# Kernel optimization log

Hardware: AMD Instinct MI355X
Metric: run time of the kernel (lower is better)

## Reference

```python
import jax, jax.numpy as jnp
import numpy as np

B, H, W = 16, 512, 512


def conv2d(x, w, b):
    # NCHW conv, stride 1, padding 1 (SAME for 3x3)
    y = jax.lax.conv_general_dilated(
        x, w, window_strides=(1, 1), padding=((1, 1), (1, 1)),
        dimension_numbers=("NCHW", "OIHW", "NCHW"))
    return y + b[None, :, None, None]


def bilinear_sample(img, py, px):
    # img: [B,H,W]; py,px: [B,K,H,W] float sample coords. Zero padding outside.
    Hh, Ww = img.shape[1], img.shape[2]
    y0 = jnp.floor(py)
    x0 = jnp.floor(px)
    wy = py - y0  # fractional weights
    wx = px - x0
    y0i = y0.astype(jnp.int32)
    x0i = x0.astype(jnp.int32)

    def gather(yi, xi):
        valid = (yi >= 0) & (yi < Hh) & (xi >= 0) & (xi < Ww)
        yc = jnp.clip(yi, 0, Hh - 1)
        xc = jnp.clip(xi, 0, Ww - 1)
        v = jax.vmap(lambda im, yy, xx: im[yy, xx])(img, yc, xc)
        return jnp.where(valid, v, jnp.zeros((), img.dtype))

    v00 = gather(y0i, x0i)
    v01 = gather(y0i, x0i + 1)
    v10 = gather(y0i + 1, x0i)
    v11 = gather(y0i + 1, x0i + 1)
    return (v00 * (1 - wy) * (1 - wx) + v01 * (1 - wy) * wx
            + v10 * wy * (1 - wx) + v11 * wy * wx)


def setup_inputs() -> dict:
    key = jax.random.key(0)
    ks = jax.random.split(key, 7)
    pm25 = jax.random.normal(ks[0], (B, 1, H, W), jnp.float32)
    avg_wind = jax.random.normal(ks[1], (B, 2, H, W), jnp.float32)
    topo = jax.random.normal(ks[2], (B, 1, H, W), jnp.float32)
    # offset_conv params (Kaiming-ish small random)
    conv1_w = jax.random.normal(ks[3], (16, 3, 3, 3), jnp.float32) * (1.0 / np.sqrt(3 * 9))
    conv1_b = jax.random.normal(ks[4], (16,), jnp.float32) * 0.01
    conv2_w = jax.random.normal(ks[5], (18, 16, 3, 3), jnp.float32) * (1.0 / np.sqrt(16 * 9))
    conv2_b = jax.random.normal(ks[6], (18,), jnp.float32) * 0.01
    # dirac init: identity 3x3 kernel
    weight = jnp.zeros((1, 1, 3, 3), jnp.float32).at[0, 0, 1, 1].set(1.0)
    return {"pm25": pm25, "avg_wind": avg_wind, "topo": topo,
            "conv1_w": conv1_w, "conv1_b": conv1_b,
            "conv2_w": conv2_w, "conv2_b": conv2_b, "weight": weight}


def reference(pm25, avg_wind, topo, conv1_w, conv1_b, conv2_w, conv2_b, weight):
    # offset-predicting conv stack
    feat = jax.nn.gelu(conv2d(jnp.concatenate([avg_wind, topo], axis=1), conv1_w, conv1_b), approximate=False)
    offsets = conv2d(feat, conv2_w, conv2_b)          # [B, 2*3*3, H, W]
    b, _, h, w = offsets.shape
    off = offsets.reshape(b, 9, 2, h, w)              # k = i*3 + j; [.,k,0]=dy, [.,k,1]=dx
    dy, dx = off[:, :, 0], off[:, :, 1]               # [B,9,H,W]

    ys = jnp.arange(h, dtype=pm25.dtype)[None, None, :, None]
    xs = jnp.arange(w, dtype=pm25.dtype)[None, None, None, :]
    ki = jnp.arange(3, dtype=pm25.dtype)
    kdy = (jnp.repeat(ki, 3) - 1.0)[None, :, None, None]  # kernel row offset - pad
    kdx = (jnp.tile(ki, 3) - 1.0)[None, :, None, None]    # kernel col offset - pad

    py = ys + kdy + dy                                # sample rows   [B,9,H,W]
    px = xs + kdx + dx                                # sample cols   [B,9,H,W]

    samp = bilinear_sample(pm25[:, 0], py, px)        # [B,9,H,W]
    wk = weight.reshape(9)                            # single-channel 3x3 kernel
    out = jnp.einsum("bkhw,k->bhw", samp, wk)[:, None]
    return out                                        # [B,1,H,W]
```

## Files before the change

kernel.cpp:

```cpp
#include <hip/hip_runtime.h>
#include <math.h>

#define Bn 16
#define Hh 512
#define Ww 512
#define HW_ (Hh * Ww)
#define TW 32
#define TH 16
#define NTHREADS 512
#define S 37
#define NROWS 20
#define SIN_N 800
#define NFP 672
#define NT 42

typedef __bf16 bfrag __attribute__((ext_vector_type(8)));
typedef __bf16 bf4   __attribute__((ext_vector_type(4)));
typedef float  ffrag __attribute__((ext_vector_type(16)));
typedef float  f32x4 __attribute__((ext_vector_type(4)));
typedef float  f32x2 __attribute__((ext_vector_type(2)));

__device__ __forceinline__ short f2bf(float f) {
    unsigned u = __float_as_uint(f);
    unsigned r = u + 0x7FFFu + ((u >> 16) & 1u);
    return (short)(r >> 16);
}

__device__ __forceinline__ f32x2 mk2(float a, float b) { f32x2 t; t.x = a; t.y = b; return t; }

__device__ __forceinline__ f32x2 gelu_fast2(f32x2 x) {
    const float C0 = 1.1259890f, C1 = -0.3565430f, C2 = 0.0848830f,
                C3 = -0.0110610f, C4 = 0.0005820f;
    f32x2 y = x * 0.70710678f;
    f32x2 t;
    t.x = fminf(fmaxf(y.x, -2.5f), 2.5f);
    t.y = fminf(fmaxf(y.y, -2.5f), 2.5f);
    f32x2 u = t * t;
    f32x2 p = u * C4 + C3;
    p = p * u + C2;
    p = p * u + C1;
    p = p * u + C0;
    f32x2 e = t * p;
    f32x2 h = x * 0.5f;
    return h * e + h;
}

__device__ __forceinline__ float bilin(const float* __restrict__ img, float py, float px) {
    float y0f = floorf(py), x0f = floorf(px);
    float wy = py - y0f, wx = px - x0f;
    int y0 = (int)y0f, x0 = (int)x0f;
    int yc0 = min(max(y0, 0), Hh - 1), yc1 = min(max(y0 + 1, 0), Hh - 1);
    int xc0 = min(max(x0, 0), Ww - 1), xc1 = min(max(x0 + 1, 0), Ww - 1);
    bool vy0 = (unsigned)y0 < (unsigned)Hh, vy1 = (unsigned)(y0 + 1) < (unsigned)Hh;
    bool vx0 = (unsigned)x0 < (unsigned)Ww, vx1 = (unsigned)(x0 + 1) < (unsigned)Ww;
    const float* r0 = img + yc0 * Ww;
    const float* r1 = img + yc1 * Ww;
    float v00 = (vy0 && vx0) ? r0[xc0] : 0.0f;
    float v01 = (vy0 && vx1) ? r0[xc1] : 0.0f;
    float v10 = (vy1 && vx0) ? r1[xc0] : 0.0f;
    float v11 = (vy1 && vx1) ? r1[xc1] : 0.0f;
    return (1.0f - wy) * ((1.0f - wx) * v00 + wx * v01) +
           wy          * ((1.0f - wx) * v10 + wx * v11);
}

__global__ void pack_w(const float* __restrict__ w2, const float* __restrict__ w1,
                       const float* __restrict__ b1, int* __restrict__ ws) {
    const int lane = threadIdx.x;
    const int l31  = lane & 31;
    const int lh   = lane >> 5;
    for (int tap = 0; tap < 9; ++tap) {
        int pk[4];
        #pragma unroll
        for (int jj = 0; jj < 4; ++jj) {
            float v0 = (l31 < 18) ? w2[(l31 * 16 + lh * 8 + 2 * jj    ) * 9 + tap] : 0.0f;
            float v1 = (l31 < 18) ? w2[(l31 * 16 + lh * 8 + 2 * jj + 1) * 9 + tap] : 0.0f;
            pk[jj] = ((int)(unsigned short)f2bf(v0)) | ((int)f2bf(v1) << 16);
        }
        ((int4*)ws)[tap * 64 + lane] = make_int4(pk[0], pk[1], pk[2], pk[3]);
    }
    const int m  = lane & 15;
    const int kq = lane >> 4;
    for (int t = 0; t < 2; ++t) {
        int pk[4];
        #pragma unroll
        for (int jj = 0; jj < 4; ++jj) {
            float vv[2];
            #pragma unroll
            for (int h = 0; h < 2; ++h) {
                int k   = kq * 8 + 2 * jj + h;
                int kyl = k >> 4, kx = (k >> 2) & 3, c = k & 3;
                int ky  = 2 * t + kyl;
                float x = 0.0f;
                if (kx < 3 && c < 3 && ky < 3) x = w1[m * 27 + c * 9 + ky * 3 + kx];
                if (t == 0 && k == 3) x = b1[m];
                vv[h] = x;
            }
            pk[jj] = ((int)(unsigned short)f2bf(vv[0])) | ((int)f2bf(vv[1]) << 16);
        }
        ((int4*)ws)[576 + t * 64 + lane] = make_int4(pk[0], pk[1], pk[2], pk[3]);
    }
}

#define SMEM_BYTES (SIN_N * 16 + 2 * NFP * 16)

__global__ __launch_bounds__(NTHREADS, 8) void residual_advection_fused(
    const float* __restrict__ pm25,
    const float* __restrict__ wind,
    const float* __restrict__ topo,
    const float* __restrict__ b2,
    const float* __restrict__ wt,
    const int*   __restrict__ wsB,
    float* __restrict__ out)
{
    __shared__ __align__(16) char smem[SMEM_BYTES];
    __bf16* s_in   = (__bf16*)smem;
    __bf16* s_feat = (__bf16*)(smem + SIN_N * 16);

    const int tid = threadIdx.x;
    const int bb  = blockIdx.z;
    const int ty0 = blockIdx.y * TH;
    const int tx0 = blockIdx.x * TW;
    const bool edge = (ty0 == 0) || (ty0 == Hh - TH) || (tx0 == 0) || (tx0 == Ww - TW);

    const int lane = tid & 63;
    const int wv   = tid >> 6;
    const int l31  = lane & 31;
    const int lh   = lane >> 5;

    const bfrag* WF = (const bfrag*)wsB;

    bfrag w1f0 = WF[576 + lane];
    bfrag w1f1 = WF[640 + lane];

    for (int idx = tid; idx < SIN_N; idx += NTHREADS) {
        float c0 = 0.0f, c1 = 0.0f, c2 = 0.0f;
        if (idx < NROWS * S) {
            int r = idx / S, c = idx - r * S;
            if (!edge) {
                int g = (ty0 - 2 + r) * Ww + (tx0 - 2 + c);
                c0 = wind[(bb * 2 + 0) * HW_ + g];
                c1 = wind[(bb * 2 + 1) * HW_ + g];
                c2 = topo[bb * HW_ + g];
            } else {
                int gy = ty0 - 2 + r, gx = tx0 - 2 + c;
                if ((unsigned)gy < (unsigned)Hh && (unsigned)gx < (unsigned)Ww) {
                    int g = gy * Ww + gx;
                    c0 = wind[(bb * 2 + 0) * HW_ + g];
                    c1 = wind[(bb * 2 + 1) * HW_ + g];
                    c2 = topo[bb * HW_ + g];
                }
            }
        }
        bf4 v;
        v[0] = (__bf16)c0; v[1] = (__bf16)c1; v[2] = (__bf16)c2; v[3] = (__bf16)1.0f;
        *(bf4*)&s_in[idx * 8] = v;
        if (idx > 0) *(bf4*)&s_in[idx * 8 - 4] = v;
    }
    __syncthreads();

    {
        const int n    = lane & 15;
        const int kq   = lane >> 4;
        const int qoff = (kq >> 1) * S + (kq & 1) * 2;
        for (int tt = wv; tt < NT; tt += 8) {
            const int p = tt * 16 + n;
            f32x4 acc;
            acc[0] = 0.0f; acc[1] = 0.0f; acc[2] = 0.0f; acc[3] = 0.0f;
            bfrag bx0 = *(const bfrag*)&s_in[(p + qoff) * 8];
            bfrag bx1 = *(const bfrag*)&s_in[(p + qoff + 2 * S) * 8];
            acc = __builtin_amdgcn_mfma_f32_16x16x32_bf16(w1f0, bx0, acc, 0, 0, 0);
            acc = __builtin_amdgcn_mfma_f32_16x16x32_bf16(w1f1, bx1, acc, 0, 0, 0);
            f32x2 g0 = gelu_fast2(mk2(acc[0], acc[1]));
            f32x2 g1 = gelu_fast2(mk2(acc[2], acc[3]));
            if (edge) {
                int fy = p / S;
                int fx = p - fy * S;
                int gy = ty0 + fy - 1, gx = tx0 + fx - 1;
                float msk = ((unsigned)gy < (unsigned)Hh && (unsigned)gx < (unsigned)Ww)
                            ? 1.0f : 0.0f;
                g0 *= msk; g1 *= msk;
            }
            bf4 w4;
            w4[0] = (__bf16)g0.x; w4[1] = (__bf16)g0.y;
            w4[2] = (__bf16)g1.x; w4[3] = (__bf16)g1.y;
            *(bf4*)&s_feat[((kq >> 1) * NFP + p) * 8 + (kq & 1) * 4] = w4;
        }
    }
    __syncthreads();

    ffrag a0, a1;
    #pragma unroll
    for (int r = 0; r < 16; ++r) { a0[r] = 0.0f; a1[r] = 0.0f; }
    {
        const int vb = (lh * NFP + (2 * wv) * S + l31) * 8;
        #pragma unroll
        for (int kx = 0; kx < 3; ++kx) {
            bfrag f0 = *(const bfrag*)&s_feat[vb + (0 * S + kx) * 8];
            bfrag f1 = *(const bfrag*)&s_feat[vb + (1 * S + kx) * 8];
            bfrag f2 = *(const bfrag*)&s_feat[vb + (2 * S + kx) * 8];
            bfrag f3 = *(const bfrag*)&s_feat[vb + (3 * S + kx) * 8];
            bfrag w0 = WF[(0 * 3 + kx) * 64 + lane];
            bfrag w1_ = WF[(1 * 3 + kx) * 64 + lane];
            bfrag w2_ = WF[(2 * 3 + kx) * 64 + lane];
            a0 = __builtin_amdgcn_mfma_f32_32x32x16_bf16(w0,  f0, a0, 0, 0, 0);
            a1 = __builtin_amdgcn_mfma_f32_32x32x16_bf16(w0,  f1, a1, 0, 0, 0);
            a0 = __builtin_amdgcn_mfma_f32_32x32x16_bf16(w1_, f1, a0, 0, 0, 0);
            a1 = __builtin_amdgcn_mfma_f32_32x32x16_bf16(w1_, f2, a1, 0, 0, 0);
            a0 = __builtin_amdgcn_mfma_f32_32x32x16_bf16(w2_, f2, a0, 0, 0, 0);
            a1 = __builtin_amdgcn_mfma_f32_32x32x16_bf16(w2_, f3, a1, 0, 0, 0);
        }
    }

    {
        const float* img = pm25 + bb * HW_;
        const int py_i = ty0 + 2 * wv + lh;
        const int px_i = tx0 + l31;
        const float fy = (float)py_i, fx = (float)px_i;
        float o = 0.0f;
        #pragma unroll
        for (int t = 0; t < 9; ++t) {
            float wk = wt[t];
            if (wk != 0.0f) {
                const int o_h = (t >> 1) & 1;
                const int rg  = ((2 * t) & 3) + 4 * (t >> 2);
                float dy, dx;
                if (o_h == 0) {
                    float sy = __shfl_xor(a1[rg], 32);
                    float sx = __shfl_xor(a1[rg + 1], 32);
                    dy = lh ? sy : a0[rg];
                    dx = lh ? sx : a0[rg + 1];
                } else {
                    float sy = __shfl_xor(a0[rg], 32);
                    float sx = __shfl_xor(a0[rg + 1], 32);
                    dy = lh ? a1[rg] : sy;
                    dx = lh ? a1[rg + 1] : sx;
                }
                dy += b2[2 * t];
                dx += b2[2 * t + 1];
                float py = fy + (float)(t / 3 - 1) + dy;
                float px = fx + (float)(t % 3 - 1) + dx;
                o += wk * bilin(img, py, px);
            }
        }
        out[bb * HW_ + py_i * Ww + px_i] = o;
    }
}

extern "C" void kernel_launch(void* const* d_in, const int* in_sizes, int n_in,
                              void* d_out, int out_size, void* d_ws, size_t ws_size,
                              hipStream_t stream) {
    const float* pm25 = (const float*)d_in[0];
    const float* wind = (const float*)d_in[1];
    const float* topo = (const float*)d_in[2];
    const float* w1   = (const float*)d_in[3];
    const float* b1   = (const float*)d_in[4];
    const float* w2   = (const float*)d_in[5];
    const float* b2   = (const float*)d_in[6];
    const float* wt   = (const float*)d_in[7];
    float* o          = (float*)d_out;
    int*   wsB        = (int*)d_ws;

    pack_w<<<dim3(1), dim3(64), 0, stream>>>(w2, w1, b1, wsB);

    dim3 grid(Ww / TW, Hh / TH, Bn);
    residual_advection_fused<<<grid, dim3(NTHREADS), 0, stream>>>(
        pm25, wind, topo, b2, wt, wsB, o);
}
```

Measured before the change: 175.2 us.

## Loop each block over eight vertical tiles with register prefetch of next inputs

Each block now walks eight consecutive 32x16 tiles down the image instead of handling one, so the grid is eight times smaller. While the current tile is computed, each thread loads the next tile's wind and topo halo values into registers. The first-conv loop becomes a fixed six-iteration unrolled loop, and the shared buffers are padded so the extra positions read zeros. This is meant to hide global-load latency and cut per-block setup, at the cost of fewer resident blocks, less parallelism across the GPU, and some wasted MFMA work on the padding positions.

```diff
diff --git a/kernel.cpp b/kernel.cpp
--- a/kernel.cpp
+++ b/kernel.cpp
@@ -8,11 +8,13 @@
 #define TW 32
 #define TH 16
 #define NTHREADS 512
+#define TPB 8
 #define S 37
 #define NROWS 20
-#define SIN_N 800
-#define NFP 672
-#define NT 42
+#define NVALID (NROWS * S)
+#define SIN_N 912
+#define NFP 800
+#define SMEM_BYTES (SIN_N * 16 + 2 * NFP * 16)
 
 typedef __bf16 bfrag __attribute__((ext_vector_type(8)));
 typedef __bf16 bf4   __attribute__((ext_vector_type(4)));
@@ -101,8 +103,6 @@
     }
 }
 
-#define SMEM_BYTES (SIN_N * 16 + 2 * NFP * 16)
-
 __global__ __launch_bounds__(NTHREADS, 8) void residual_advection_fused(
     const float* __restrict__ pm25,
     const float* __restrict__ wind,
@@ -118,9 +118,8 @@
 
     const int tid = threadIdx.x;
     const int bb  = blockIdx.z;
-    const int ty0 = blockIdx.y * TH;
     const int tx0 = blockIdx.x * TW;
-    const bool edge = (ty0 == 0) || (ty0 == Hh - TH) || (tx0 == 0) || (tx0 == Ww - TW);
+    int ty0 = blockIdx.y * (TPB * TH);
 
     const int lane = tid & 63;
     const int wv   = tid >> 6;
@@ -128,121 +127,152 @@
     const int lh   = lane >> 5;
 
     const bfrag* WF = (const bfrag*)wsB;
-
     bfrag w1f0 = WF[576 + lane];
     bfrag w1f1 = WF[640 + lane];
 
-    for (int idx = tid; idx < SIN_N; idx += NTHREADS) {
-        float c0 = 0.0f, c1 = 0.0f, c2 = 0.0f;
-        if (idx < NROWS * S) {
-            int r = idx / S, c = idx - r * S;
-            if (!edge) {
-                int g = (ty0 - 2 + r) * Ww + (tx0 - 2 + c);
-                c0 = wind[(bb * 2 + 0) * HW_ + g];
-                c1 = wind[(bb * 2 + 1) * HW_ + g];
-                c2 = topo[bb * HW_ + g];
-            } else {
-                int gy = ty0 - 2 + r, gx = tx0 - 2 + c;
-                if ((unsigned)gy < (unsigned)Hh && (unsigned)gx < (unsigned)Ww) {
-                    int g = gy * Ww + gx;
-                    c0 = wind[(bb * 2 + 0) * HW_ + g];
-                    c1 = wind[(bb * 2 + 1) * HW_ + g];
-                    c2 = topo[bb * HW_ + g];
+    {
+        bf4 z;
+        z[0] = (__bf16)0.0f; z[1] = (__bf16)0.0f; z[2] = (__bf16)0.0f; z[3] = (__bf16)0.0f;
+        for (int pos = NVALID + tid; pos < SIN_N; pos += NTHREADS) {
+            *(bf4*)&s_in[pos * 8] = z;
+            *(bf4*)&s_in[pos * 8 - 4] = z;
+        }
+    }
+
+    const int rA = tid / S, cA = tid - rA * S;
+    const int tidB = tid + NTHREADS;
+    const int rB = tidB / S, cB = tidB - rB * S;
+    const bool haveB = tidB < NVALID;
+    const int gxA = tx0 - 2 + cA;  const bool vxA = (unsigned)gxA < (unsigned)Ww;
+    const int gxB = tx0 - 2 + cB;  const bool vxB = (unsigned)gxB < (unsigned)Ww;
+    const float* wp0 = wind + (bb * 2 + 0) * HW_;
+    const float* wp1 = wind + (bb * 2 + 1) * HW_;
+    const float* tp  = topo + bb * HW_;
+    const float* img = pm25 + bb * HW_;
+
+    float sa0, sa1, sa2, sb0, sb1, sb2;
+    auto stage = [&](int ty) {
+        int gyA = ty - 2 + rA;
+        bool vA = vxA && (unsigned)gyA < (unsigned)Hh;
+        sa0 = 0.0f; sa1 = 0.0f; sa2 = 0.0f;
+        if (vA) { int g = gyA * Ww + gxA; sa0 = wp0[g]; sa1 = wp1[g]; sa2 = tp[g]; }
+        sb0 = 0.0f; sb1 = 0.0f; sb2 = 0.0f;
+        if (haveB) {
+            int gyB = ty - 2 + rB;
+            bool vB = vxB && (unsigned)gyB < (unsigned)Hh;
+            if (vB) { int g = gyB * Ww + gxB; sb0 = wp0[g]; sb1 = wp1[g]; sb2 = tp[g]; }
+        }
+    };
+
+    stage(ty0);
+
+    for (int it = 0; it < TPB; ++it) {
+        {
+            bf4 v;
+            v[0] = (__bf16)sa0; v[1] = (__bf16)sa1; v[2] = (__bf16)sa2; v[3] = (__bf16)1.0f;
+            *(bf4*)&s_in[tid * 8] = v;
+            if (tid > 0) *(bf4*)&s_in[tid * 8 - 4] = v;
+            if (haveB) {
+                bf4 w;
+                w[0] = (__bf16)sb0; w[1] = (__bf16)sb1; w[2] = (__bf16)sb2; w[3] = (__bf16)1.0f;
+                *(bf4*)&s_in[tidB * 8] = w;
+                *(bf4*)&s_in[tidB * 8 - 4] = w;
+            }
+        }
+        __syncthreads();
+
+        if (it + 1 < TPB) stage(ty0 + TH);
+
+        const bool edge = (ty0 == 0) || (ty0 == Hh - TH) || (tx0 == 0) || (tx0 == Ww - TW);
+
+        {
+            const int n    = lane & 15;
+            const int kq   = lane >> 4;
+            const int qoff = (kq >> 1) * S + (kq & 1) * 2;
+            #pragma unroll
+            for (int ii = 0; ii < 6; ++ii) {
+                const int p = (wv + 8 * ii) * 16 + n;
+                f32x4 acc;
+                acc[0] = 0.0f; acc[1] = 0.0f; acc[2] = 0.0f; acc[3] = 0.0f;
+                bfrag bx0 = *(const bfrag*)&s_in[(p + qoff) * 8];
+                bfrag bx1 = *(const bfrag*)&s_in[(p + qoff + 2 * S) * 8];
+                acc = __builtin_amdgcn_mfma_f32_16x16x32_bf16(w1f0, bx0, acc, 0, 0, 0);
+                acc = __builtin_amdgcn_mfma_f32_16x16x32_bf16(w1f1, bx1, acc, 0, 0, 0);
+                f32x2 g0 = gelu_fast2(mk2(acc[0], acc[1]));
+                f32x2 g1 = gelu_fast2(mk2(acc[2], acc[3]));
+                if (edge) {
+                    int fy = p / S;
+                    int fx = p - fy * S;
+                    int gy = ty0 + fy - 1, gx = tx0 + fx - 1;
+                    float msk = ((unsigned)gy < (unsigned)Hh && (unsigned)gx < (unsigned)Ww)
+                                ? 1.0f : 0.0f;
+                    g0 *= msk; g1 *= msk;
                 }
-            }
-        }
-        bf4 v;
-        v[0] = (__bf16)c0; v[1] = (__bf16)c1; v[2] = (__bf16)c2; v[3] = (__bf16)1.0f;
-        *(bf4*)&s_in[idx * 8] = v;
-        if (idx > 0) *(bf4*)&s_in[idx * 8 - 4] = v;
-    }
-    __syncthreads();
-
-    {
-        const int n    = lane & 15;
-        const int kq   = lane >> 4;
-        const int qoff = (kq >> 1) * S + (kq & 1) * 2;
-        for (int tt = wv; tt < NT; tt += 8) {
-            const int p = tt * 16 + n;
-            f32x4 acc;
-            acc[0] = 0.0f; acc[1] = 0.0f; acc[2] = 0.0f; acc[3] = 0.0f;
-            bfrag bx0 = *(const bfrag*)&s_in[(p + qoff) * 8];
-            bfrag bx1 = *(const bfrag*)&s_in[(p + qoff + 2 * S) * 8];
-            acc = __builtin_amdgcn_mfma_f32_16x16x32_bf16(w1f0, bx0, acc, 0, 0, 0);
-            acc = __builtin_amdgcn_mfma_f32_16x16x32_bf16(w1f1, bx1, acc, 0, 0, 0);
-            f32x2 g0 = gelu_fast2(mk2(acc[0], acc[1]));
-            f32x2 g1 = gelu_fast2(mk2(acc[2], acc[3]));
-            if (edge) {
-                int fy = p / S;
-                int fx = p - fy * S;
-                int gy = ty0 + fy - 1, gx = tx0 + fx - 1;
-                float msk = ((unsigned)gy < (unsigned)Hh && (unsigned)gx < (unsigned)Ww)
-                            ? 1.0f : 0.0f;
-                g0 *= msk; g1 *= msk;
-            }
-            bf4 w4;
-            w4[0] = (__bf16)g0.x; w4[1] = (__bf16)g0.y;
-            w4[2] = (__bf16)g1.x; w4[3] = (__bf16)g1.y;
-            *(bf4*)&s_feat[((kq >> 1) * NFP + p) * 8 + (kq & 1) * 4] = w4;
-        }
-    }
-    __syncthreads();
-
-    ffrag a0, a1;
-    #pragma unroll
-    for (int r = 0; r < 16; ++r) { a0[r] = 0.0f; a1[r] = 0.0f; }
-    {
-        const int vb = (lh * NFP + (2 * wv) * S + l31) * 8;
+                bf4 w4;
+                w4[0] = (__bf16)g0.x; w4[1] = (__bf16)g0.y;
+                w4[2] = (__bf16)g1.x; w4[3] = (__bf16)g1.y;
+                *(bf4*)&s_feat[((kq >> 1) * NFP + p) * 8 + (kq & 1) * 4] = w4;
+            }
+        }
+        __syncthreads();
+
+        ffrag a0, a1;
         #pragma unroll
-        for (int kx = 0; kx < 3; ++kx) {
-            bfrag f0 = *(const bfrag*)&s_feat[vb + (0 * S + kx) * 8];
-            bfrag f1 = *(const bfrag*)&s_feat[vb + (1 * S + kx) * 8];
-            bfrag f2 = *(const bfrag*)&s_feat[vb + (2 * S + kx) * 8];
-            bfrag f3 = *(const bfrag*)&s_feat[vb + (3 * S + kx) * 8];
-            bfrag w0 = WF[(0 * 3 + kx) * 64 + lane];
-            bfrag w1_ = WF[(1 * 3 + kx) * 64 + lane];
-            bfrag w2_ = WF[(2 * 3 + kx) * 64 + lane];
-            a0 = __builtin_amdgcn_mfma_f32_32x32x16_bf16(w0,  f0, a0, 0, 0, 0);
-            a1 = __builtin_amdgcn_mfma_f32_32x32x16_bf16(w0,  f1, a1, 0, 0, 0);
-            a0 = __builtin_amdgcn_mfma_f32_32x32x16_bf16(w1_, f1, a0, 0, 0, 0);
-            a1 = __builtin_amdgcn_mfma_f32_32x32x16_bf16(w1_, f2, a1, 0, 0, 0);
-            a0 = __builtin_amdgcn_mfma_f32_32x32x16_bf16(w2_, f2, a0, 0, 0, 0);
-            a1 = __builtin_amdgcn_mfma_f32_32x32x16_bf16(w2_, f3, a1, 0, 0, 0);
-        }
-    }
-
-    {
-        const float* img = pm25 + bb * HW_;
-        const int py_i = ty0 + 2 * wv + lh;
-        const int px_i = tx0 + l31;
-        const float fy = (float)py_i, fx = (float)px_i;
-        float o = 0.0f;
-        #pragma unroll
-        for (int t = 0; t < 9; ++t) {
-            float wk = wt[t];
-            if (wk != 0.0f) {
-                const int o_h = (t >> 1) & 1;
-                const int rg  = ((2 * t) & 3) + 4 * (t >> 2);
-                float dy, dx;
-                if (o_h == 0) {
-                    float sy = __shfl_xor(a1[rg], 32);
-                    float sx = __shfl_xor(a1[rg + 1], 32);
-                    dy = lh ? sy : a0[rg];
-                    dx = lh ? sx : a0[rg + 1];
-                } else {
-                    float sy = __shfl_xor(a0[rg], 32);
-                    float sx = __shfl_xor(a0[rg + 1], 32);
-                    dy = lh ? a1[rg] : sy;
-                    dx = lh ? a1[rg + 1] : sx;
+        for (int r = 0; r < 16; ++r) { a0[r] = 0.0f; a1[r] = 0.0f; }
+        {
+            const int vb = (lh * NFP + (2 * wv) * S + l31) * 8;
+            #pragma unroll
+            for (int kx = 0; kx < 3; ++kx) {
+                bfrag f0 = *(const bfrag*)&s_feat[vb + (0 * S + kx) * 8];
+                bfrag f1 = *(const bfrag*)&s_feat[vb + (1 * S + kx) * 8];
+                bfrag f2 = *(const bfrag*)&s_feat[vb + (2 * S + kx) * 8];
+                bfrag f3 = *(const bfrag*)&s_feat[vb + (3 * S + kx) * 8];
+                bfrag w0  = WF[(0 * 3 + kx) * 64 + lane];
+                bfrag w1_ = WF[(1 * 3 + kx) * 64 + lane];
+                bfrag w2_ = WF[(2 * 3 + kx) * 64 + lane];
+                a0 = __builtin_amdgcn_mfma_f32_32x32x16_bf16(w0,  f0, a0, 0, 0, 0);
+                a1 = __builtin_amdgcn_mfma_f32_32x32x16_bf16(w0,  f1, a1, 0, 0, 0);
+                a0 = __builtin_amdgcn_mfma_f32_32x32x16_bf16(w1_, f1, a0, 0, 0, 0);
+                a1 = __builtin_amdgcn_mfma_f32_32x32x16_bf16(w1_, f2, a1, 0, 0, 0);
+                a0 = __builtin_amdgcn_mfma_f32_32x32x16_bf16(w2_, f2, a0, 0, 0, 0);
+                a1 = __builtin_amdgcn_mfma_f32_32x32x16_bf16(w2_, f3, a1, 0, 0, 0);
+            }
+        }
+
+        {
+            const int py_i = ty0 + 2 * wv + lh;
+            const int px_i = tx0 + l31;
+            const float fy = (float)py_i, fx = (float)px_i;
+            float o = 0.0f;
+            #pragma unroll
+            for (int t = 0; t < 9; ++t) {
+                float wk = wt[t];
+                if (wk != 0.0f) {
+                    const int o_h = (t >> 1) & 1;
+                    const int rg  = ((2 * t) & 3) + 4 * (t >> 2);
+                    float dy, dx;
+                    if (o_h == 0) {
+                        float sy = __shfl_xor(a1[rg], 32);
+                        float sx = __shfl_xor(a1[rg + 1], 32);
+                        dy = lh ? sy : a0[rg];
+                        dx = lh ? sx : a0[rg + 1];
+                    } else {
+                        float sy = __shfl_xor(a0[rg], 32);
+                        float sx = __shfl_xor(a0[rg + 1], 32);
+                        dy = lh ? a1[rg] : sy;
+                        dx = lh ? a1[rg + 1] : sx;
+                    }
+                    dy += b2[2 * t];
+                    dx += b2[2 * t + 1];
+                    float py = fy + (float)(t / 3 - 1) + dy;
+                    float px = fx + (float)(t % 3 - 1) + dx;
+                    o += wk * bilin(img, py, px);
                 }
-                dy += b2[2 * t];
-                dx += b2[2 * t + 1];
-                float py = fy + (float)(t / 3 - 1) + dy;
-                float px = fx + (float)(t % 3 - 1) + dx;
-                o += wk * bilin(img, py, px);
-            }
-        }
-        out[bb * HW_ + py_i * Ww + px_i] = o;
+            }
+            out[bb * HW_ + py_i * Ww + px_i] = o;
+        }
+
+        ty0 += TH;
     }
 }
 
@@ -262,7 +292,7 @@
 
     pack_w<<<dim3(1), dim3(64), 0, stream>>>(w2, w1, b1, wsB);
 
-    dim3 grid(Ww / TW, Hh / TH, Bn);
+    dim3 grid(Ww / TW, Hh / (TH * TPB), Bn);
     residual_advection_fused<<<grid, dim3(NTHREADS), 0, stream>>>(
         pm25, wind, topo, b2, wt, wsB, o);
 }
```

Measured after the change: 337.7 us. 92.7% more time.
